# Kernel tuning notes

Measured on AMD Instinct MI355X. Metric: run time of the kernel, lower is better.

Reference implementation:

```python
import jax, jax.numpy as jnp
import numpy as np


def _conv(x, w, b, s):
    # x: NCHW, w: OIHW, VALID padding, stride s
    y = jax.lax.conv_general_dilated(x, w, (s, s), 'VALID',
                                     dimension_numbers=('NCHW', 'OIHW', 'NCHW'))
    return y + b[None, :, None, None]


def _deconv(x, w, b, s):
    # PyTorch ConvTranspose2d (weight IOHW, padding=0): conv of input dilated by s
    # with spatially-flipped, in/out-swapped kernel and full padding k-1.
    k = w.shape[2]
    wk = jnp.flip(w, (2, 3)).transpose(1, 0, 2, 3)  # -> OIHW
    y = jax.lax.conv_general_dilated(x, wk, (1, 1), [(k - 1, k - 1), (k - 1, k - 1)],
                                     lhs_dilation=(s, s),
                                     dimension_numbers=('NCHW', 'OIHW', 'NCHW'))
    return y + b[None, :, None, None]


def setup_inputs() -> dict:
    key = jax.random.key(0)
    ks = iter(jax.random.split(key, 40))
    def p(shape, scale=0.05):
        return jax.random.normal(next(ks), shape, jnp.float32) * scale
    return dict(
        x=jax.random.normal(next(ks), (50, 1, 64, 64), jnp.float32),
        action=jax.random.normal(next(ks), (50, 30), jnp.float32),
        h0=jax.random.normal(next(ks), (50, 1024), jnp.float32),
        c0=jax.random.normal(next(ks), (50, 1024), jnp.float32),
        conv1_w=p((32, 1, 4, 4)), conv1_b=p((32,)),
        conv2_w=p((64, 32, 4, 4)), conv2_b=p((64,)),
        conv3_w=p((128, 64, 4, 4)), conv3_b=p((128,)),
        conv4_w=p((256, 128, 4, 4)), conv4_b=p((256,)),
        fc1_w=p((482, 1024)), fc1_b=p((482,)),
        fc2_w=p((1024, 512)), fc2_b=p((1024,)),
        w_ih=p((4096, 1024)), w_hh=p((4096, 1024)),
        b_ih=p((4096,)), b_hh=p((4096,)),
        fcsd_w=p((1024, 1024)), fcsd_b=p((1024,)),
        d1_w=p((1024, 128, 5, 5)), d1_b=p((128,)),
        d2_w=p((128, 64, 5, 5)), d2_b=p((64,)),
        d3_w=p((64, 32, 6, 6)), d3_b=p((32,)),
        d4_w=p((32, 1, 6, 6)), d4_b=p((1,)),
        fc5_w=p((1, 512)), fc5_b=p((1,)),
    )


def reference(x, action, h0, c0,
              conv1_w, conv1_b, conv2_w, conv2_b, conv3_w, conv3_b, conv4_w, conv4_b,
              fc1_w, fc1_b, fc2_w, fc2_b,
              w_ih, w_hh, b_ih, b_hh,
              fcsd_w, fcsd_b,
              d1_w, d1_b, d2_w, d2_b, d3_w, d3_b, d4_w, d4_b,
              fc5_w, fc5_b):
    B = x.shape[0]  # 50 (hardcoded in original)
    T = 17          # PHYRE_MAX_TIMESTEPS
    h = x
    for w, b in ((conv1_w, conv1_b), (conv2_w, conv2_b), (conv3_w, conv3_b), (conv4_w, conv4_b)):
        h = jnp.tanh(_conv(h, w, b, 2))
    flat = h.reshape(B, -1)                      # [50, 1024]
    fc1 = flat @ fc1_w.T + fc1_b                 # [50, 482]
    z = jnp.concatenate([fc1, action], axis=1)   # [50, 512]
    fc2_out = jax.nn.leaky_relu(z @ fc2_w.T + fc2_b)  # [50, 1024]

    def step(carry, _):
        xt, hs, cs = carry
        g = xt @ w_ih.T + b_ih + hs @ w_hh.T + b_hh   # [B, 4096], gates i,f,g,o
        i, f, gg, o = jnp.split(g, 4, axis=1)
        cs = jax.nn.sigmoid(f) * cs + jax.nn.sigmoid(i) * jnp.tanh(gg)
        hs = jax.nn.sigmoid(o) * jnp.tanh(cs)
        return (hs, hs, cs), hs  # output fed back as next input

    _, outs = jax.lax.scan(step, (fc2_out, h0, c0), None, length=T)  # [17, 50, 1024]
    hd = jax.nn.leaky_relu(jnp.einsum('tbd,ed->tbe', outs, fcsd_w) + fcsd_b)
    hd = hd.reshape(T * B, 1024, 1, 1)  # t-major flatten, matching torch .view
    y = jnp.tanh(_deconv(hd, d1_w, d1_b, 2))   # [850,128,5,5]
    y = jnp.tanh(_deconv(y, d2_w, d2_b, 2))    # [850,64,13,13]
    y = jnp.tanh(_deconv(y, d3_w, d3_b, 2))    # [850,32,30,30]
    y = _deconv(y, d4_w, d4_b, 2)              # [850,1,64,64]
    obs = y.reshape(B, T, 1, 64, 64)  # faithful to original's view (layout quirk)
    reward = z @ fc5_w.T + fc5_b      # [50, 1]
    return obs, reward
```

## Files before the change

### kernel.cpp

```cpp
#include <hip/hip_runtime.h>
#include <math.h>

#define DI __device__ __forceinline__

DI float sigm(float x){ return 1.0f/(1.0f+expf(-x)); }
DI float lrelu(float x){ return x > 0.f ? x : 0.01f*x; }

template<int ACT>
DI float act_apply(float v){
    if (ACT == 1) return tanhf(v);
    if (ACT == 2) return lrelu(v);
    return v;
}

template<int CIN, int COUT>
__global__ __launch_bounds__(256)
void conv_enc_kernel(const float* __restrict__ in, const float* __restrict__ w,
                     const float* __restrict__ bias, float* __restrict__ out,
                     int N, int H, int OH)
{
    int idx = blockIdx.x*256 + threadIdx.x;
    int total = N*COUT*OH*OH;
    if (idx >= total) return;
    int ox = idx % OH; int t = idx / OH;
    int oy = t % OH;   t /= OH;
    int o  = t % COUT; int n = t / COUT;
    float acc = bias[o];
    const float* wp = w + o*CIN*16;
    const float* ip = in + ((size_t)n*CIN)*H*H + (oy*2)*H + ox*2;
    for (int c = 0; c < CIN; ++c) {
        const float* ipc = ip + c*H*H;
        const float* wpc = wp + c*16;
        #pragma unroll
        for (int ky = 0; ky < 4; ++ky)
            #pragma unroll
            for (int kx = 0; kx < 4; ++kx)
                acc = fmaf(ipc[ky*H + kx], wpc[ky*4 + kx], acc);
    }
    out[idx] = tanhf(acc);
}

template<int BM,int BN,int BK,bool BT,int ACT>
__global__ __launch_bounds__((BM/4)*(BN/4))
void gemm_kernel(const float* __restrict__ A, const float* __restrict__ Bm,
                 const float* __restrict__ bias, float* __restrict__ C,
                 int M, int N, int Kfull, int klen, int ldc, int bias_div,
                 long partStride)
{
    constexpr int TM = 4, TN = 4;
    constexpr int THREADS = (BM/TM)*(BN/TN);
    constexpr int LDA = BM + 4, LDB = BN + 4;
    __shared__ __align__(16) float As[BK][LDA];
    __shared__ __align__(16) float Bs[BK][LDB];
    int tid = threadIdx.x;
    int m0 = blockIdx.y * BM, n0 = blockIdx.x * BN;
    int koff = blockIdx.z * klen;
    C += (long)blockIdx.z * partStride;
    constexpr int NTX = BN/TN;
    int tx = tid % NTX, ty = tid / NTX;
    float acc[4][4];
    #pragma unroll
    for (int i=0;i<4;++i)
        #pragma unroll
        for (int j=0;j<4;++j) acc[i][j] = 0.f;

    for (int k0 = 0; k0 < klen; k0 += BK) {
        for (int e = tid; e < BM*BK; e += THREADS) {
            int k = e % BK, m = e / BK;
            As[k][m] = (m0+m < M) ? A[(size_t)(m0+m)*Kfull + koff + k0 + k] : 0.f;
        }
        if (BT) {
            for (int e = tid; e < BN*BK; e += THREADS) {
                int k = e % BK, n = e / BK;
                Bs[k][n] = (n0+n < N) ? Bm[(size_t)(n0+n)*Kfull + koff + k0 + k] : 0.f;
            }
        } else {
            for (int e = tid; e < BN*BK; e += THREADS) {
                int n = e % BN, k = e / BN;
                Bs[k][n] = (n0+n < N) ? Bm[(size_t)(koff + k0 + k)*N + n0+n] : 0.f;
            }
        }
        __syncthreads();
        #pragma unroll 8
        for (int k = 0; k < BK; ++k) {
            float4 a4 = *reinterpret_cast<const float4*>(&As[k][ty*4]);
            float4 b4 = *reinterpret_cast<const float4*>(&Bs[k][tx*4]);
            float av[4] = {a4.x, a4.y, a4.z, a4.w};
            float bv[4] = {b4.x, b4.y, b4.z, b4.w};
            #pragma unroll
            for (int i=0;i<4;++i)
                #pragma unroll
                for (int j=0;j<4;++j)
                    acc[i][j] = fmaf(av[i], bv[j], acc[i][j]);
        }
        __syncthreads();
    }
    #pragma unroll
    for (int i=0;i<4;++i) {
        int m = m0 + ty*4 + i;
        if (m >= M) continue;
        #pragma unroll
        for (int j=0;j<4;++j) {
            int n = n0 + tx*4 + j;
            if (n >= N) continue;
            float v = acc[i][j] + (bias ? bias[n / bias_div] : 0.f);
            C[(size_t)m*ldc + n] = act_apply<ACT>(v);
        }
    }
}

__global__ __launch_bounds__(256)
void addvec_kernel(const float* __restrict__ a, const float* __restrict__ b,
                   float* __restrict__ o, int n)
{
    int i = blockIdx.x*256 + threadIdx.x;
    if (i < n) o[i] = a[i] + b[i];
}

__global__ __launch_bounds__(64)
void concat_action_kernel(const float* __restrict__ action, float* __restrict__ z)
{
    int i = blockIdx.x*64 + threadIdx.x;
    if (i < 50*30) { int b = i/30, k = i%30; z[b*512 + 482 + k] = action[i]; }
}

__global__ __launch_bounds__(64)
void reward_kernel(const float* __restrict__ z, const float* __restrict__ w,
                   const float* __restrict__ b, float* __restrict__ out)
{
    int bi = threadIdx.x;
    if (bi < 50) {
        float acc = b[0];
        for (int k = 0; k < 512; ++k) acc = fmaf(z[bi*512 + k], w[k], acc);
        out[bi] = acc;
    }
}

__global__ __launch_bounds__(256)
void lstm_gates16_kernel(const float* __restrict__ gp, const float* __restrict__ bsum,
                         const float* __restrict__ c_prev,
                         float* __restrict__ c_out, float* __restrict__ h_out,
                         float* __restrict__ outs_t)
{
    int idx = blockIdx.x*256 + threadIdx.x;
    if (idx >= 50*1024) return;
    int b = idx >> 10, j = idx & 1023;
    float s0 = bsum[j], s1 = bsum[1024+j], s2 = bsum[2048+j], s3 = bsum[3072+j];
    #pragma unroll
    for (int p = 0; p < 16; ++p) {
        const float* base = gp + (size_t)p*204800 + b*4096 + j;
        s0 += base[0]; s1 += base[1024]; s2 += base[2048]; s3 += base[3072];
    }
    float cp = c_prev[idx];
    float c = sigm(s1)*cp + sigm(s0)*tanhf(s2);
    float h = sigm(s3)*tanhf(c);
    c_out[idx] = c; h_out[idx] = h; outs_t[idx] = h;
}

__global__ __launch_bounds__(256)
void wprep_kernel(const float* __restrict__ w, float* __restrict__ wp,
                  int CIN, int COUT, int KS)
{
    int idx = blockIdx.x*256 + threadIdx.x;
    int total = 4*CIN*COUT*12;
    if (idx >= total) return;
    int slot = idx % 12; int rem = idx / 12;
    int o = rem % COUT; rem /= COUT;
    int c = rem % CIN;  int pp = rem / CIN;
    int py = pp >> 1, px = pp & 1;
    int j = slot >> 2, i = slot & 3;
    int ky = py + 2*j, kx = px + 2*i;
    float v = 0.f;
    if (i < 3 && ky < KS && kx < KS)
        v = w[(((size_t)c*COUT + o)*KS + ky)*KS + kx];
    wp[idx] = v;
}

template<int CIN,int COUT,int HIN,int HOUT,int ACT,int VSPLIT,int ROWP,int TWU,
         int VPER,int TB,int MWAVES>
__global__ __launch_bounds__(256, MWAVES)
void deconv4_kernel(const float* __restrict__ in, const float* __restrict__ wp,
                    const float* __restrict__ bias, float* __restrict__ out)
{
    constexpr int NV = (HOUT + 1) / 2;
    constexpr int NVSEG = (NV + VSPLIT - 1) / VSPLIT;
    constexpr int NVB = (NVSEG + VPER - 1) / VPER;
    constexpr int ROWS_MAX = NVSEG + 2;
    constexpr int NR4 = (TWU + 2 + 3) / 4;
    constexpr int RLEN = (TWU == 1) ? 4 : NR4*4;
    static_assert(NVB * COUT * TB <= 256, "tasks must fit one per thread");
    __shared__ __align__(16) float slab[CIN*ROWS_MAX*ROWP];

    int n   = blockIdx.x / VSPLIT;
    int seg = blockIdx.x % VSPLIT;
    int v0 = seg * NVSEG;
    int v1 = (v0 + NVSEG < NV) ? v0 + NVSEG : NV;
    int r0 = (v0 - 2 > 0) ? v0 - 2 : 0;
    int r1m = (v1 - 1 < HIN - 1) ? v1 - 1 : HIN - 1;
    int nrows = r1m - r0 + 1;
    int tid = threadIdx.x;
    const float* inb = in + (size_t)n*CIN*HIN*HIN;
    const size_t PPSTR = (size_t)CIN*COUT*12;

    for (int e = tid; e < CIN*ROWS_MAX; e += 256) {
        int c = e / ROWS_MAX, ri = e % ROWS_MAX;
        if (ri < nrows) {
            const float* src = inb + ((size_t)c*HIN + r0 + ri)*HIN;
            float* dst = slab + (c*ROWS_MAX + ri)*ROWP;
            dst[0] = 0.f; dst[1] = 0.f;
            #pragma unroll
            for (int x2 = HIN+2; x2 < ROWP; ++x2) dst[x2] = 0.f;
            for (int x2 = 0; x2 < HIN; ++x2) dst[2+x2] = src[x2];
        }
    }
    __syncthreads();

    int task = tid;
    int vi = task % NVB; int rem = task / NVB;
    int o = rem % COUT;  int tb = rem / COUT;
    int u0 = tb * TWU;
    bool anyv = false;
    int vg[VPER];
    #pragma unroll
    for (int q = 0; q < VPER; ++q) {
        vg[q] = v0 + vi + q*NVB;
        if (vg[q] < v1) anyv = true;
    }
    if (tb >= TB) anyv = false;

    float acc[VPER][2][2][TWU];
    #pragma unroll
    for (int q=0;q<VPER;++q)
        #pragma unroll
        for (int a=0;a<2;++a)
            #pragma unroll
            for (int b=0;b<2;++b)
                #pragma unroll
                for (int t=0;t<TWU;++t) acc[q][a][b][t] = 0.f;

    if (anyv) {
        const float* wb0 = wp + ((size_t)0*COUT + o)*12;
        for (int c = 0; c < CIN; ++c) {
            const float* wbase = wb0 + (size_t)c*COUT*12;
            const float* sc = slab + c*(ROWS_MAX*ROWP);
            #pragma unroll
            for (int jj = 0; jj < 3; ++jj) {
                float r[VPER][RLEN];
                #pragma unroll
                for (int q = 0; q < VPER; ++q) {
                    int iy = vg[q] - jj;
                    if (iy >= 0 && iy < HIN) {
                        const float* srow = sc + (iy - r0)*ROWP + u0;
                        if constexpr (TWU == 1) {
                            r[q][0] = srow[0]; r[q][1] = srow[1]; r[q][2] = srow[2];
                        } else {
                            #pragma unroll
                            for (int p4 = 0; p4 < NR4; ++p4) {
                                float4 f = *reinterpret_cast<const float4*>(srow + p4*4);
                                r[q][p4*4]=f.x; r[q][p4*4+1]=f.y; r[q][p4*4+2]=f.z; r[q][p4*4+3]=f.w;
                            }
                        }
                    } else {
                        #pragma unroll
                        for (int p4 = 0; p4 < RLEN; ++p4) r[q][p4] = 0.f;
                    }
                }
                #pragma unroll
                for (int pp = 0; pp < 4; ++pp) {
                    float4 w4 = *reinterpret_cast<const float4*>(wbase + pp*PPSTR + jj*4);
                    int py = pp >> 1, px = pp & 1;
                    #pragma unroll
                    for (int q = 0; q < VPER; ++q)
                        #pragma unroll
                        for (int t = 0; t < TWU; ++t)
                            acc[q][py][px][t] =
                                fmaf(w4.x, r[q][t+2],
                                fmaf(w4.y, r[q][t+1],
                                fmaf(w4.z, r[q][t], acc[q][py][px][t])));
                }
            }
        }
        float bv = bias[o];
        #pragma unroll
        for (int q = 0; q < VPER; ++q) {
            if (vg[q] >= v1) continue;
            #pragma unroll
            for (int py = 0; py < 2; ++py) {
                int y = py + 2*vg[q];
                if (y >= HOUT) continue;
                float* ob = out + (((size_t)n*COUT + o)*HOUT + y)*HOUT;
                #pragma unroll
                for (int t = 0; t < TWU; ++t) {
                    int x0 = 2*(u0+t);
                    if (x0 + 1 < HOUT) {
                        float2 qv;
                        qv.x = act_apply<ACT>(acc[q][py][0][t] + bv);
                        qv.y = act_apply<ACT>(acc[q][py][1][t] + bv);
                        *reinterpret_cast<float2*>(ob + x0) = qv;
                    } else if (x0 < HOUT) {
                        ob[x0] = act_apply<ACT>(acc[q][py][0][t] + bv);
                    }
                }
            }
        }
    }
}

extern "C" void kernel_launch(void* const* d_in, const int* in_sizes, int n_in,
                              void* d_out, int out_size, void* d_ws, size_t ws_size,
                              hipStream_t stream)
{
    const float* x       = (const float*)d_in[0];
    const float* action  = (const float*)d_in[1];
    const float* h0      = (const float*)d_in[2];
    const float* c0      = (const float*)d_in[3];
    const float* conv1_w = (const float*)d_in[4];  const float* conv1_b = (const float*)d_in[5];
    const float* conv2_w = (const float*)d_in[6];  const float* conv2_b = (const float*)d_in[7];
    const float* conv3_w = (const float*)d_in[8];  const float* conv3_b = (const float*)d_in[9];
    const float* conv4_w = (const float*)d_in[10]; const float* conv4_b = (const float*)d_in[11];
    const float* fc1_w   = (const float*)d_in[12]; const float* fc1_b   = (const float*)d_in[13];
    const float* fc2_w   = (const float*)d_in[14]; const float* fc2_b   = (const float*)d_in[15];
    const float* w_ih    = (const float*)d_in[16]; const float* w_hh    = (const float*)d_in[17];
    const float* b_ih    = (const float*)d_in[18]; const float* b_hh    = (const float*)d_in[19];
    const float* fcsd_w  = (const float*)d_in[20]; const float* fcsd_b  = (const float*)d_in[21];
    const float* d1_w    = (const float*)d_in[22]; const float* d1_b    = (const float*)d_in[23];
    const float* d2_w    = (const float*)d_in[24]; const float* d2_b    = (const float*)d_in[25];
    const float* d3_w    = (const float*)d_in[26]; const float* d3_b    = (const float*)d_in[27];
    const float* d4_w    = (const float*)d_in[28]; const float* d4_b    = (const float*)d_in[29];
    const float* fc5_w   = (const float*)d_in[30]; const float* fc5_b   = (const float*)d_in[31];
    float* out = (float*)d_out;
    float* ws  = (float*)d_ws;

    float* a1   = ws;
    float* a2   = a1 + 1537600;
    float* a3   = a2 + 627200;
    float* flat = a3 + 230400;
    float* z    = flat + 51200;
    float* fc2o = z + 25600;
    float* hbuf = fc2o + 51200;
    float* cbuf = hbuf + 51200;
    float* outs = cbuf + 51200;
    float* hd   = outs + 870400;
    float* wsum = hd + 870400;
    float* bsum = wsum + 4194304;
    float* wp2  = bsum + 4096;
    float* wp3  = wp2 + 393216;
    float* wp4  = wp3 + 98304;
    float* y1   = wp4 + 1536;
    float* y2   = y1 + 2720000;
    float* y3   = y2 + 9193600;
    float* g16  = y1;

    const int B = 50;
    const long GP = 204800;

    addvec_kernel<<<(4194304+255)/256, 256, 0, stream>>>(w_ih, w_hh, wsum, 4194304);
    addvec_kernel<<<(4096+255)/256, 256, 0, stream>>>(b_ih, b_hh, bsum, 4096);
    wprep_kernel<<<(4*128*64*12+255)/256, 256, 0, stream>>>(d2_w, wp2, 128, 64, 5);
    wprep_kernel<<<(4*64*32*12+255)/256, 256, 0, stream>>>(d3_w, wp3, 64, 32, 6);
    wprep_kernel<<<(4*32*1*12+255)/256, 256, 0, stream>>>(d4_w, wp4, 32, 1, 6);

    conv_enc_kernel<1,32><<<(B*32*31*31+255)/256, 256, 0, stream>>>(x, conv1_w, conv1_b, a1, B, 64, 31);
    conv_enc_kernel<32,64><<<(B*64*14*14+255)/256, 256, 0, stream>>>(a1, conv2_w, conv2_b, a2, B, 31, 14);
    conv_enc_kernel<64,128><<<(B*128*6*6+255)/256, 256, 0, stream>>>(a2, conv3_w, conv3_b, a3, B, 14, 6);
    conv_enc_kernel<128,256><<<(B*256*2*2+255)/256, 256, 0, stream>>>(a3, conv4_w, conv4_b, flat, B, 6, 2);

    {
        dim3 grid((482+63)/64, (B+31)/32, 1);
        gemm_kernel<32,64,32,true,0><<<grid, 128, 0, stream>>>(flat, fc1_w, fc1_b, z, B, 482, 1024, 1024, 512, 1, 0);
    }
    concat_action_kernel<<<(1500+63)/64, 64, 0, stream>>>(action, z);
    reward_kernel<<<1, 64, 0, stream>>>(z, fc5_w, fc5_b, out + (size_t)850*4096);

    {
        dim3 grid((1024+63)/64, (B+31)/32, 1);
        gemm_kernel<32,64,32,true,2><<<grid, 128, 0, stream>>>(z, fc2_w, fc2_b, fc2o, B, 1024, 512, 512, 1024, 1, 0);
    }

    {
        dim3 grid0(64, 2, 8);
        gemm_kernel<32,64,32,true,0><<<grid0, 128, 0, stream>>>(fc2o, w_ih, nullptr, g16, B, 4096, 1024, 128, 4096, 1, GP);
        gemm_kernel<32,64,32,true,0><<<grid0, 128, 0, stream>>>(h0, w_hh, nullptr, g16 + 8*GP, B, 4096, 1024, 128, 4096, 1, GP);
        lstm_gates16_kernel<<<200, 256, 0, stream>>>(g16, bsum, c0, cbuf, hbuf, outs);
        dim3 gridt(64, 2, 16);
        for (int t = 1; t < 17; ++t) {
            gemm_kernel<32,64,32,true,0><<<gridt, 128, 0, stream>>>(hbuf, wsum, nullptr, g16, B, 4096, 1024, 64, 4096, 1, GP);
            lstm_gates16_kernel<<<200, 256, 0, stream>>>(g16, bsum, cbuf, cbuf, hbuf, outs + (size_t)t*51200);
        }
    }

    {
        dim3 grid((1024+63)/64, (850+63)/64, 1);
        gemm_kernel<64,64,32,true,2><<<grid, 256, 0, stream>>>(outs, fcsd_w, fcsd_b, hd, 850, 1024, 1024, 1024, 1024, 1, 0);
    }
    {
        dim3 grid((3200+63)/64, (850+63)/64, 1);
        gemm_kernel<64,64,32,false,1><<<grid, 256, 0, stream>>>(hd, d1_w, d1_b, y1, 850, 3200, 1024, 1024, 3200, 25, 0);
    }

    deconv4_kernel<128,64,5,13,1, 1,12,7,2,1,4><<<850, 256, 0, stream>>>(y1, wp2, d2_b, y2);
    deconv4_kernel<64,32,13,30,1, 2,20,15,1,1,3><<<1700, 256, 0, stream>>>(y2, wp3, d3_b, y3);
    deconv4_kernel<32,1,30,64,0, 4,36,1,1,32,3><<<3400, 256, 0, stream>>>(y3, wp4, d4_b, out);

    (void)in_sizes; (void)n_in; (void)out_size; (void)ws_size;
}
```

Before: 3.035 ms.

## Pad deconv intermediate row strides, retune deconv tiling, halve LSTM split-K

Deconv intermediates are now stored with padded row strides (16 and 32 floats) via new input and output stride template parameters, which should allow aligned row access. The d3 deconv tiling is retuned (TWU 8, VPER 2, TB 2) and the d2 deconv wave hint drops from 4 to 3. The LSTM recurrent GEMM split-K goes from 16 to 8 partitions, so the gate kernel sums fewer partials at the cost of fewer GEMM blocks. The padded buffers enlarge the workspace layout, and y3 is shifted to fit.

```diff
diff --git a/kernel.cpp b/kernel.cpp
--- a/kernel.cpp
+++ b/kernel.cpp
@@ -137,17 +137,17 @@
 }
 
 __global__ __launch_bounds__(256)
-void lstm_gates16_kernel(const float* __restrict__ gp, const float* __restrict__ bsum,
-                         const float* __restrict__ c_prev,
-                         float* __restrict__ c_out, float* __restrict__ h_out,
-                         float* __restrict__ outs_t)
+void lstm_gates8_kernel(const float* __restrict__ gp, const float* __restrict__ bsum,
+                        const float* __restrict__ c_prev,
+                        float* __restrict__ c_out, float* __restrict__ h_out,
+                        float* __restrict__ outs_t)
 {
     int idx = blockIdx.x*256 + threadIdx.x;
     if (idx >= 50*1024) return;
     int b = idx >> 10, j = idx & 1023;
     float s0 = bsum[j], s1 = bsum[1024+j], s2 = bsum[2048+j], s3 = bsum[3072+j];
     #pragma unroll
-    for (int p = 0; p < 16; ++p) {
+    for (int p = 0; p < 8; ++p) {
         const float* base = gp + (size_t)p*204800 + b*4096 + j;
         s0 += base[0]; s1 += base[1024]; s2 += base[2048]; s3 += base[3072];
     }
@@ -177,7 +177,7 @@
 }
 
 template<int CIN,int COUT,int HIN,int HOUT,int ACT,int VSPLIT,int ROWP,int TWU,
-         int VPER,int TB,int MWAVES>
+         int VPER,int TB,int MWAVES,int ISTR,int OSTR>
 __global__ __launch_bounds__(256, MWAVES)
 void deconv4_kernel(const float* __restrict__ in, const float* __restrict__ wp,
                     const float* __restrict__ bias, float* __restrict__ out)
@@ -185,7 +185,7 @@
     constexpr int NV = (HOUT + 1) / 2;
     constexpr int NVSEG = (NV + VSPLIT - 1) / VSPLIT;
     constexpr int NVB = (NVSEG + VPER - 1) / VPER;
-    constexpr int ROWS_MAX = NVSEG + 2;
+    constexpr int ROWS_MAX = (NVSEG + 2 < HIN) ? (NVSEG + 2) : HIN;
     constexpr int NR4 = (TWU + 2 + 3) / 4;
     constexpr int RLEN = (TWU == 1) ? 4 : NR4*4;
     static_assert(NVB * COUT * TB <= 256, "tasks must fit one per thread");
@@ -199,13 +199,13 @@
     int r1m = (v1 - 1 < HIN - 1) ? v1 - 1 : HIN - 1;
     int nrows = r1m - r0 + 1;
     int tid = threadIdx.x;
-    const float* inb = in + (size_t)n*CIN*HIN*HIN;
+    const float* inb = in + (size_t)n*CIN*HIN*ISTR;
     const size_t PPSTR = (size_t)CIN*COUT*12;
 
     for (int e = tid; e < CIN*ROWS_MAX; e += 256) {
         int c = e / ROWS_MAX, ri = e % ROWS_MAX;
         if (ri < nrows) {
-            const float* src = inb + ((size_t)c*HIN + r0 + ri)*HIN;
+            const float* src = inb + ((size_t)c*HIN + r0 + ri)*ISTR;
             float* dst = slab + (c*ROWS_MAX + ri)*ROWP;
             dst[0] = 0.f; dst[1] = 0.f;
             #pragma unroll
@@ -239,7 +239,7 @@
                 for (int t=0;t<TWU;++t) acc[q][a][b][t] = 0.f;
 
     if (anyv) {
-        const float* wb0 = wp + ((size_t)0*COUT + o)*12;
+        const float* wb0 = wp + (size_t)o*12;
         for (int c = 0; c < CIN; ++c) {
             const float* wbase = wb0 + (size_t)c*COUT*12;
             const float* sc = slab + c*(ROWS_MAX*ROWP);
@@ -288,7 +288,7 @@
             for (int py = 0; py < 2; ++py) {
                 int y = py + 2*vg[q];
                 if (y >= HOUT) continue;
-                float* ob = out + (((size_t)n*COUT + o)*HOUT + y)*HOUT;
+                float* ob = out + (((size_t)n*COUT + o)*HOUT + y)*OSTR;
                 #pragma unroll
                 for (int t = 0; t < TWU; ++t) {
                     int x0 = 2*(u0+t);
@@ -348,8 +348,8 @@
     float* wp4  = wp3 + 98304;
     float* y1   = wp4 + 1536;
     float* y2   = y1 + 2720000;
-    float* y3   = y2 + 9193600;
-    float* g16  = y1;
+    float* y3   = y2 + 11315200;
+    float* g8   = y1;
 
     const int B = 50;
     const long GP = 204800;
@@ -378,14 +378,14 @@
     }
 
     {
-        dim3 grid0(64, 2, 8);
-        gemm_kernel<32,64,32,true,0><<<grid0, 128, 0, stream>>>(fc2o, w_ih, nullptr, g16, B, 4096, 1024, 128, 4096, 1, GP);
-        gemm_kernel<32,64,32,true,0><<<grid0, 128, 0, stream>>>(h0, w_hh, nullptr, g16 + 8*GP, B, 4096, 1024, 128, 4096, 1, GP);
-        lstm_gates16_kernel<<<200, 256, 0, stream>>>(g16, bsum, c0, cbuf, hbuf, outs);
-        dim3 gridt(64, 2, 16);
+        dim3 grid0(64, 2, 4);
+        gemm_kernel<32,64,32,true,0><<<grid0, 128, 0, stream>>>(fc2o, w_ih, nullptr, g8, B, 4096, 1024, 256, 4096, 1, GP);
+        gemm_kernel<32,64,32,true,0><<<grid0, 128, 0, stream>>>(h0, w_hh, nullptr, g8 + 4*GP, B, 4096, 1024, 256, 4096, 1, GP);
+        lstm_gates8_kernel<<<200, 256, 0, stream>>>(g8, bsum, c0, cbuf, hbuf, outs);
+        dim3 gridt(64, 2, 8);
         for (int t = 1; t < 17; ++t) {
-            gemm_kernel<32,64,32,true,0><<<gridt, 128, 0, stream>>>(hbuf, wsum, nullptr, g16, B, 4096, 1024, 64, 4096, 1, GP);
-            lstm_gates16_kernel<<<200, 256, 0, stream>>>(g16, bsum, cbuf, cbuf, hbuf, outs + (size_t)t*51200);
+            gemm_kernel<32,64,32,true,0><<<gridt, 128, 0, stream>>>(hbuf, wsum, nullptr, g8, B, 4096, 1024, 128, 4096, 1, GP);
+            lstm_gates8_kernel<<<200, 256, 0, stream>>>(g8, bsum, cbuf, cbuf, hbuf, outs + (size_t)t*51200);
         }
     }
 
@@ -398,9 +398,9 @@
         gemm_kernel<64,64,32,false,1><<<grid, 256, 0, stream>>>(hd, d1_w, d1_b, y1, 850, 3200, 1024, 1024, 3200, 25, 0);
     }
 
-    deconv4_kernel<128,64,5,13,1, 1,12,7,2,1,4><<<850, 256, 0, stream>>>(y1, wp2, d2_b, y2);
-    deconv4_kernel<64,32,13,30,1, 2,20,15,1,1,3><<<1700, 256, 0, stream>>>(y2, wp3, d3_b, y3);
-    deconv4_kernel<32,1,30,64,0, 4,36,1,1,32,3><<<3400, 256, 0, stream>>>(y3, wp4, d4_b, out);
+    deconv4_kernel<128,64,5,13,1, 1,12,7,2,1,3, 5,16><<<850, 256, 0, stream>>>(y1, wp2, d2_b, y2);
+    deconv4_kernel<64,32,13,30,1, 2,20,8,2,2,3, 16,32><<<1700, 256, 0, stream>>>(y2, wp3, d3_b, y3);
+    deconv4_kernel<32,1,30,64,0, 4,36,1,1,32,3, 32,64><<<3400, 256, 0, stream>>>(y3, wp4, d4_b, out);
 
     (void)in_sizes; (void)n_in; (void)out_size; (void)ws_size;
 }
```

New measurement: 3.448 ms. 13.6% more time.
